# Performance work log

Hardware: AMD Instinct MI355X
Metric: run time of the kernel (lower is better)

## Reference

```python
import jax, jax.numpy as jnp
import numpy as np

NEG_SLOPE = 0.1
BN_EPS = 1e-5
STD_EPS = 1e-5


def leaky_relu(x):
    return jnp.where(x >= 0, x, NEG_SLOPE * x)


def conv_bn_act(x, w, gamma, beta):
    # Conv1d(kernel_size=1, bias=False) + BatchNorm1d (train-mode batch stats) + LeakyReLU(0.1)
    y = jnp.einsum('bcn,oc->bon', x, w)
    m = y.mean(axis=(0, 2), keepdims=True)
    v = y.var(axis=(0, 2), keepdims=True)  # biased, as torch BN
    y = (y - m) / jnp.sqrt(v + BN_EPS) * gamma[None, :, None] + beta[None, :, None]
    return leaky_relu(y)


def knn_idx(x, k):
    # x: [B, C, N]; faithful to torch knn(): topk(k+1) of negative squared distance, then keep first k (includes self)
    xx = jnp.sum(x * x, axis=1, keepdims=True)            # [B, 1, N]
    inner = -2.0 * jnp.einsum('bcn,bcm->bnm', x, x)       # [B, N, N]
    pd = -xx - inner - jnp.swapaxes(xx, 1, 2)             # [B, N, N]
    _, idx = jax.lax.top_k(pd, k + 1)
    return idx[:, :, :k]


def setup_inputs() -> dict:
    key = jax.random.key(0)
    ks = jax.random.split(key, 4)
    B, C, N, O = 8, 3, 4096, 32
    return {
        'xyz': jax.random.normal(ks[0], (B, C, N), dtype=jnp.float32),
        'w_nn': jax.random.normal(ks[1], (O, C), dtype=jnp.float32) * 0.1,
        'alpha': jnp.ones((1, 1, 1, O), dtype=jnp.float32),
        'beta_a': jnp.zeros((1, 1, 1, O), dtype=jnp.float32),
        'w0': jax.random.normal(ks[2], (O, C), dtype=jnp.float32) * 0.1,
        'g0': jnp.ones((O,), dtype=jnp.float32),
        'b0': jnp.zeros((O,), dtype=jnp.float32),
        'w1': jax.random.normal(ks[3], (O, O), dtype=jnp.float32) * 0.1,
        'g1': jnp.ones((O,), dtype=jnp.float32),
        'b1': jnp.zeros((O,), dtype=jnp.float32),
        'k': 16,
    }


def reference(xyz, w_nn, alpha, beta_a, w0, g0, b0, w1, g1, b1, k):
    # MLP branch on raw channels
    x = conv_bn_act(xyz, w0, g0, b0)
    x = conv_bn_act(x, w1, g1, b1)          # [B, 32, N]

    # KNN + gather neighbors
    idx = knn_idx(xyz, k)                   # [B, N, k]
    pts = jnp.swapaxes(xyz, 1, 2)           # [B, N, C]
    grouped = jax.vmap(lambda p, i: p[i])(pts, idx)  # [B, N, k, C]

    # neighbor_normal: diff -> 1x1 conv -> global-std normalize -> affine
    res = grouped - pts[:, :, None, :]
    res = jnp.einsum('bnkc,oc->bnko', res, w_nn)      # [B, N, k, 32]
    B = res.shape[0]
    std = jnp.std(res.reshape(B, -1), axis=-1, ddof=1).reshape(B, 1, 1, 1)  # torch.std is unbiased
    gp = alpha * (res / (std + STD_EPS)) + beta_a

    # max over neighbors, to [B, 32, N]
    gp = jnp.swapaxes(gp.max(axis=2), 1, 2)

    point_feature = jnp.concatenate([x, gp], axis=1)  # [B, 64, N]
    return point_feature, idx
```

## Files before the change

### kernel.cpp

```cpp
#include <hip/hip_runtime.h>
#include <stdint.h>

#define B_  8
#define N_  4096
#define O_  32
#define K_  16
#define BN_ (B_ * N_)
#define PF_ (B_ * 64 * N_)
#define CB_ 256
#define RPB 4
#define CHK 512
#define NCHK (N_ / CHK)

enum : int {
  WS_PARTA = 0,
  WS_XX    = 1024,
  WS_SC0   = WS_XX + BN_,
  WS_SH0   = WS_SC0 + 32,
  WS_PARTC = WS_SH0 + 32,
  WS_SC1   = WS_PARTC + 4096,
  WS_SH1   = WS_SC1 + 32,
  WS_MAXV  = WS_SH1 + 32,
  WS_MINV  = WS_MAXV + BN_ * 32,
  WS_ROWS  = WS_MINV + BN_ * 32,
  WS_DEN   = WS_ROWS + BN_ * 2,
  WS_TOTAL = WS_DEN + 8
};
#define WS_PARTC2 WS_MAXV

__global__ __launch_bounds__(256) void kA(const float* __restrict__ xyz,
                                          float* __restrict__ ws) {
  int tid = threadIdx.x;
  int gid = blockIdx.x * 256 + tid;
  float s0 = 0.f, s1 = 0.f, s2 = 0.f;
  float m00 = 0.f, m01 = 0.f, m02 = 0.f, m11 = 0.f, m12 = 0.f, m22 = 0.f;
  for (int i = gid; i < BN_; i += 64 * 256) {
    int b = i >> 12, n = i & (N_ - 1);
    const float* xb = xyz + b * 3 * N_;
    float x0 = xb[n], x1 = xb[N_ + n], x2 = xb[2 * N_ + n];
    float xx = __fadd_rn(__fadd_rn(__fmul_rn(x0, x0), __fmul_rn(x1, x1)),
                         __fmul_rn(x2, x2));
    ws[WS_XX + i] = xx;
    s0 += x0; s1 += x1; s2 += x2;
    m00 = fmaf(x0, x0, m00); m01 = fmaf(x0, x1, m01); m02 = fmaf(x0, x2, m02);
    m11 = fmaf(x1, x1, m11); m12 = fmaf(x1, x2, m12); m22 = fmaf(x2, x2, m22);
  }
  __shared__ float sd[256];
  float acc[9] = {s0, s1, s2, m00, m01, m02, m11, m12, m22};
#pragma unroll
  for (int q = 0; q < 9; ++q) {
    sd[tid] = acc[q];
    __syncthreads();
    for (int s = 128; s > 0; s >>= 1) {
      if (tid < s) sd[tid] += sd[tid + s];
      __syncthreads();
    }
    if (tid == 0) ws[WS_PARTA + blockIdx.x * 9 + q] = sd[0];
    __syncthreads();
  }
}

__global__ __launch_bounds__(64) void kB(const float* __restrict__ w0,
                                         const float* __restrict__ g0,
                                         const float* __restrict__ b0,
                                         float* __restrict__ ws) {
  __shared__ float S[9];
  int tid = threadIdx.x;
  if (tid < 9) {
    float s = 0.f;
    for (int blk = 0; blk < 64; ++blk) s += ws[WS_PARTA + blk * 9 + tid];
    S[tid] = s;
  }
  __syncthreads();
  if (tid < 32) {
    const float inv = 1.0f / 32768.0f;
    float mc0 = S[0] * inv, mc1 = S[1] * inv, mc2 = S[2] * inv;
    float M00 = S[3] * inv, M01 = S[4] * inv, M02 = S[5] * inv;
    float M11 = S[6] * inv, M12 = S[7] * inv, M22 = S[8] * inv;
    float w0c = w0[tid * 3], w1c = w0[tid * 3 + 1], w2c = w0[tid * 3 + 2];
    float m = w0c * mc0 + w1c * mc1 + w2c * mc2;
    float e2 = w0c * w0c * M00 + w1c * w1c * M11 + w2c * w2c * M22 +
               2.f * (w0c * w1c * M01 + w0c * w2c * M02 + w1c * w2c * M12);
    float v = fmaxf(e2 - m * m, 0.f);
    float sc = g0[tid] / sqrtf(v + 1e-5f);
    ws[WS_SC0 + tid] = sc;
    ws[WS_SH0 + tid] = b0[tid] - m * sc;
  }
}

__global__ __launch_bounds__(256) void kC(const float* __restrict__ xyz,
                                          const float* __restrict__ w0,
                                          const float* __restrict__ w1,
                                          float* __restrict__ ws) {
  __shared__ float w0s[96], sc0s[32], sh0s[32], w1s[32 * 33], xs[8][33], red[256];
  int tid = threadIdx.x;
  if (tid < 96) w0s[tid] = w0[tid];
  if (tid < 32) { sc0s[tid] = ws[WS_SC0 + tid]; sh0s[tid] = ws[WS_SH0 + tid]; }
  for (int i = tid; i < 1024; i += 256) w1s[(i >> 5) * 33 + (i & 31)] = w1[i];
  __syncthreads();
  int p = tid >> 5, o = tid & 31;
  float S = 0.f, S2 = 0.f;
  for (int it = 0; it < 16; ++it) {
    int i = blockIdx.x * 128 + it * 8 + p;
    int b = i >> 12, n = i & (N_ - 1);
    const float* xb = xyz + b * 3 * N_;
    float x0 = xb[n], x1 = xb[N_ + n], x2 = xb[2 * N_ + n];
    float y0 = x0 * w0s[o * 3] + x1 * w0s[o * 3 + 1] + x2 * w0s[o * 3 + 2];
    float a = y0 * sc0s[o] + sh0s[o];
    xs[p][o] = (a >= 0.f) ? a : 0.1f * a;
    __syncthreads();
    float y1 = 0.f;
#pragma unroll
    for (int c = 0; c < 32; ++c) y1 = fmaf(w1s[o * 33 + c], xs[p][c], y1);
    S += y1; S2 = fmaf(y1, y1, S2);
    __syncthreads();
  }
  red[tid] = S;
  __syncthreads();
  if (p == 0) {
    float t = 0.f;
    for (int pp = 0; pp < 8; ++pp) t += red[pp * 32 + o];
    ws[WS_PARTC2 + blockIdx.x * 64 + o] = t;
  }
  __syncthreads();
  red[tid] = S2;
  __syncthreads();
  if (p == 0) {
    float t = 0.f;
    for (int pp = 0; pp < 8; ++pp) t += red[pp * 32 + o];
    ws[WS_PARTC2 + blockIdx.x * 64 + 32 + o] = t;
  }
}

__global__ __launch_bounds__(64) void kD(const float* __restrict__ g1,
                                         const float* __restrict__ b1,
                                         float* __restrict__ ws) {
  int o = threadIdx.x;
  if (o >= 32) return;
  float S = 0.f, S2 = 0.f;
  for (int blk = 0; blk < CB_; ++blk) {
    S += ws[WS_PARTC2 + blk * 64 + o];
    S2 += ws[WS_PARTC2 + blk * 64 + 32 + o];
  }
  float m = S / 32768.f;
  float v = fmaxf(S2 / 32768.f - m * m, 0.f);
  float sc = g1[o] / sqrtf(v + 1e-5f);
  ws[WS_SC1 + o] = sc;
  ws[WS_SH1 + o] = b1[o] - m * sc;
}

__global__ __launch_bounds__(256) void kE(const float* __restrict__ xyz,
                                          const float* __restrict__ w0,
                                          const float* __restrict__ w1,
                                          const float* __restrict__ ws,
                                          float* __restrict__ out) {
  __shared__ float w0s[96], sc0s[32], sh0s[32], sc1s[32], sh1s[32], w1s[32 * 33],
      xs[8][33];
  int tid = threadIdx.x;
  if (tid < 96) w0s[tid] = w0[tid];
  if (tid < 32) {
    sc0s[tid] = ws[WS_SC0 + tid]; sh0s[tid] = ws[WS_SH0 + tid];
    sc1s[tid] = ws[WS_SC1 + tid]; sh1s[tid] = ws[WS_SH1 + tid];
  }
  for (int i = tid; i < 1024; i += 256) w1s[(i >> 5) * 33 + (i & 31)] = w1[i];
  __syncthreads();
  int p = tid >> 5, o = tid & 31;
  int o2 = tid >> 3, p2 = tid & 7;
  for (int it = 0; it < 16; ++it) {
    int i = blockIdx.x * 128 + it * 8 + p;
    int b = i >> 12, n = i & (N_ - 1);
    const float* xb = xyz + b * 3 * N_;
    float x0 = xb[n], x1 = xb[N_ + n], x2 = xb[2 * N_ + n];
    float y0 = x0 * w0s[o * 3] + x1 * w0s[o * 3 + 1] + x2 * w0s[o * 3 + 2];
    float a = y0 * sc0s[o] + sh0s[o];
    xs[p][o] = (a >= 0.f) ? a : 0.1f * a;
    __syncthreads();
    float y1 = 0.f;
#pragma unroll
    for (int c = 0; c < 32; ++c) y1 = fmaf(w1s[o * 33 + c], xs[p][c], y1);
    float z = y1 * sc1s[o] + sh1s[o];
    float x1v = (z >= 0.f) ? z : 0.1f * z;
    __syncthreads();
    xs[p][o] = x1v;
    __syncthreads();
    int i2 = blockIdx.x * 128 + it * 8 + p2;
    int b2 = i2 >> 12, n2 = i2 & (N_ - 1);
    out[b2 * 64 * N_ + o2 * N_ + n2] = xs[p2][o2];
    __syncthreads();
  }
}

__global__ __launch_bounds__(256) void kF(const float* __restrict__ xyz,
                                          const float* __restrict__ w_nn,
                                          float* __restrict__ out,
                                          float* __restrict__ ws) {
  int tid = threadIdx.x;
  int wave = tid >> 6, lane = tid & 63;
  int row = blockIdx.x * RPB + wave;
  int b = row >> 12, n = row & (N_ - 1);
  const float* xb = xyz + b * 3 * N_;
  const float* xxp = ws + WS_XX + b * N_;
  float qx = xb[n], qy = xb[N_ + n], qz = xb[2 * N_ + n];
  float xxn = xxp[n];

  __shared__ float sx[2][CHK], sy[2][CHK], sz[2][CHK], sxx[2][CHK];
  __shared__ unsigned long long list[RPB][64];
  __shared__ float rb[RPB][16][33];

  float keys[64];
  float mn = __builtin_inff();
  float rx0, rx1, ry0, ry1, rz0, rz1, rw0, rw1;
  rx0 = xb[tid];           rx1 = xb[tid + 256];
  ry0 = xb[N_ + tid];      ry1 = xb[N_ + tid + 256];
  rz0 = xb[2 * N_ + tid];  rz1 = xb[2 * N_ + tid + 256];
  rw0 = xxp[tid];          rw1 = xxp[tid + 256];
#pragma unroll
  for (int c = 0; c < NCHK; ++c) {
    int buf = c & 1;
    sx[buf][tid] = rx0;  sx[buf][tid + 256] = rx1;
    sy[buf][tid] = ry0;  sy[buf][tid + 256] = ry1;
    sz[buf][tid] = rz0;  sz[buf][tid + 256] = rz1;
    sxx[buf][tid] = rw0; sxx[buf][tid + 256] = rw1;
    __syncthreads();
    if (c + 1 < NCHK) {
      int i0 = (c + 1) * CHK + tid;
      rx0 = xb[i0];           rx1 = xb[i0 + 256];
      ry0 = xb[N_ + i0];      ry1 = xb[N_ + i0 + 256];
      rz0 = xb[2 * N_ + i0];  rz1 = xb[2 * N_ + i0 + 256];
      rw0 = xxp[i0];          rw1 = xxp[i0 + 256];
    }
#pragma unroll
    for (int jj = 0; jj < CHK / 64; ++jj) {
      int ml = (jj << 6) | lane;
      float px = sx[buf][ml], py = sy[buf][ml], pz = sz[buf][ml];
      float dot = __fmaf_rn(pz, qz, __fmaf_rn(py, qy, __fmul_rn(px, qx)));
      float inner = __fmul_rn(-2.0f, dot);
      float t = __fsub_rn(-sxx[buf][ml], inner);
      float pn = __fsub_rn(xxn, t);
      keys[c * (CHK / 64) + jj] = pn;
      mn = fminf(mn, pn);
    }
    __syncthreads();
  }

  unsigned e;
  {
    unsigned u = __float_as_uint(mn);
    u ^= ((unsigned)((int)u >> 31)) | 0x80000000u;
    e = u;
  }
#pragma unroll
  for (int k = 2; k <= 64; k <<= 1) {
#pragma unroll
    for (int d = k >> 1; d >= 1; d >>= 1) {
      unsigned pe = __shfl_xor(e, d, 64);
      bool up = ((lane & k) == 0);
      bool lower = ((lane & d) == 0);
      unsigned lo = (e < pe) ? e : pe;
      unsigned hi = (e < pe) ? pe : e;
      e = (up == lower) ? lo : hi;
    }
  }
  unsigned tm = __shfl(e, 15, 64);
  unsigned tfu = (tm & 0x80000000u) ? (tm ^ 0x80000000u) : ~tm;
  float T = __uint_as_float(tfu);

  list[wave][lane] = ~0ull;
  __syncthreads();
  int base = 0;
#pragma unroll
  for (int j = 0; j < 64; ++j) {
    bool pred = (keys[j] <= T);
    unsigned long long mask = __ballot(pred);
    if (mask != 0ull) {
      if (pred) {
        unsigned uu = __float_as_uint(keys[j]);
        uu ^= ((unsigned)((int)uu >> 31)) | 0x80000000u;
        int rank = __popcll(mask & ((1ull << lane) - 1ull));
        int slot = base + rank;
        if (slot < 64)
          list[wave][slot] = ((unsigned long long)uu << 32) |
                             (unsigned)((j << 6) | lane);
      }
      base += __popcll(mask);
    }
  }
  __syncthreads();

  unsigned long long ev = list[wave][lane];
#pragma unroll
  for (int k = 2; k <= 64; k <<= 1) {
#pragma unroll
    for (int d = k >> 1; d >= 1; d >>= 1) {
      unsigned long long pe = __shfl_xor(ev, d, 64);
      bool up = ((lane & k) == 0);
      bool lower = ((lane & d) == 0);
      bool lt = (ev < pe);
      unsigned long long lo = lt ? ev : pe;
      unsigned long long hi = lt ? pe : ev;
      ev = (up == lower) ? lo : hi;
    }
  }
  int m = (int)(unsigned)(ev & 0xffffffffull);
  if (lane < 16) out[PF_ + row * 16 + lane] = (float)m;

  float s = 0.f, s2 = 0.f;
  if (lane < 16) {
    float dx = __fsub_rn(xb[m], qx);
    float dy = __fsub_rn(xb[N_ + m], qy);
    float dz = __fsub_rn(xb[2 * N_ + m], qz);
#pragma unroll
    for (int o = 0; o < 32; ++o) {
      float r = __fmaf_rn(dz, w_nn[o * 3 + 2],
                __fmaf_rn(dy, w_nn[o * 3 + 1], __fmul_rn(dx, w_nn[o * 3])));
      rb[wave][lane][o] = r;
      s += r;
      s2 = __fmaf_rn(r, r, s2);
    }
  }
  __syncthreads();
  if (lane < 32) {
    float mx = -__builtin_inff(), mnv = __builtin_inff();
#pragma unroll
    for (int r = 0; r < 16; ++r) {
      float v = rb[wave][r][lane];
      mx = fmaxf(mx, v);
      mnv = fminf(mnv, v);
    }
    ws[WS_MAXV + row * 32 + lane] = mx;
    ws[WS_MINV + row * 32 + lane] = mnv;
  }
#pragma unroll
  for (int off = 1; off < 64; off <<= 1) {
    s += __shfl_xor(s, off, 64);
    s2 += __shfl_xor(s2, off, 64);
  }
  if (lane == 0) {
    ws[WS_ROWS + row * 2] = s;
    ws[WS_ROWS + row * 2 + 1] = s2;
  }
}

__global__ __launch_bounds__(256) void kG(float* __restrict__ ws) {
  int b = blockIdx.x, tid = threadIdx.x;
  float s = 0.f, s2 = 0.f;
  for (int i = tid; i < N_; i += 256) {
    s += ws[WS_ROWS + (b * N_ + i) * 2];
    s2 += ws[WS_ROWS + (b * N_ + i) * 2 + 1];
  }
  __shared__ float sd[256], sd2[256];
  sd[tid] = s; sd2[tid] = s2;
  __syncthreads();
  for (int st = 128; st > 0; st >>= 1) {
    if (tid < st) { sd[tid] += sd[tid + st]; sd2[tid] += sd2[tid + st]; }
    __syncthreads();
  }
  if (tid == 0) {
    const float M = 2097152.0f;
    float var = fmaxf((sd2[0] - sd[0] * (sd[0] / M)) / (M - 1.0f), 0.f);
    ws[WS_DEN + b] = sqrtf(var) + 1e-5f;
  }
}

__global__ __launch_bounds__(256) void kH(const float* __restrict__ alpha,
                                          const float* __restrict__ beta,
                                          const float* __restrict__ ws,
                                          float* __restrict__ out) {
  int i = blockIdx.x * 256 + threadIdx.x;
  if (i >= B_ * 32 * N_) return;
  int n = i & (N_ - 1);
  int o = (i >> 12) & 31;
  int b = i >> 17;
  float denom = ws[WS_DEN + b];
  float al = alpha[o], be = beta[o];
  int base = (b * N_ + n) * 32 + o;
  float v = (al >= 0.f) ? ws[WS_MAXV + base] : ws[WS_MINV + base];
  out[b * 64 * N_ + (32 + o) * N_ + n] = __fadd_rn(__fmul_rn(al, v / denom), be);
}

extern "C" void kernel_launch(void* const* d_in, const int* in_sizes, int n_in,
                              void* d_out, int out_size, void* d_ws, size_t ws_size,
                              hipStream_t stream) {
  const float* xyz   = (const float*)d_in[0];
  const float* w_nn  = (const float*)d_in[1];
  const float* alpha = (const float*)d_in[2];
  const float* beta_a= (const float*)d_in[3];
  const float* w0    = (const float*)d_in[4];
  const float* g0    = (const float*)d_in[5];
  const float* b0    = (const float*)d_in[6];
  const float* w1    = (const float*)d_in[7];
  const float* g1    = (const float*)d_in[8];
  const float* b1    = (const float*)d_in[9];
  float* out = (float*)d_out;
  float* ws  = (float*)d_ws;

  kA<<<64, 256, 0, stream>>>(xyz, ws);
  kB<<<1, 64, 0, stream>>>(w0, g0, b0, ws);
  kC<<<CB_, 256, 0, stream>>>(xyz, w0, w1, ws);
  kD<<<1, 64, 0, stream>>>(g1, b1, ws);
  kE<<<CB_, 256, 0, stream>>>(xyz, w0, w1, ws, out);
  kF<<<BN_ / RPB, RPB * 64, 0, stream>>>(xyz, w_nn, out, ws);
  kG<<<B_, 256, 0, stream>>>(ws);
  kH<<<(B_ * 32 * N_ + 255) / 256, 256, 0, stream>>>(alpha, beta_a, ws, out);
}
```

Baseline: 155.9 us.

## Fold tiny reduction kernels into consumers and process two KNN rows per wave

Removes the single-block kernels kB, kD and kG by having each consuming block recompute the BN scale/shift or the per-batch std from the partial sums, cutting launch count from eight to five. The KNN kernel now handles two query rows per wave (RPB 8 with 256 threads), so each shared-memory candidate point is reused for two distance computations. The cost is redundant reduction work in every block of kC, kE and kH, and doubled key registers per lane (128 floats), which may lower occupancy or cause spills.

Result: slower. 187.3 us (+20.1%).

```diff
diff --git a/kernel.cpp b/kernel.cpp
--- a/kernel.cpp
+++ b/kernel.cpp
@@ -8,7 +8,7 @@
 #define BN_ (B_ * N_)
 #define PF_ (B_ * 64 * N_)
 #define CB_ 256
-#define RPB 4
+#define RPB 8
 #define CHK 512
 #define NCHK (N_ / CHK)
 
@@ -60,43 +60,38 @@
   }
 }
 
-__global__ __launch_bounds__(64) void kB(const float* __restrict__ w0,
-                                         const float* __restrict__ g0,
-                                         const float* __restrict__ b0,
-                                         float* __restrict__ ws) {
-  __shared__ float S[9];
+__global__ __launch_bounds__(256) void kC(const float* __restrict__ xyz,
+                                          const float* __restrict__ w0,
+                                          const float* __restrict__ g0,
+                                          const float* __restrict__ b0,
+                                          const float* __restrict__ w1,
+                                          float* __restrict__ ws) {
+  __shared__ float S9[9];
+  __shared__ float w0s[96], sc0s[32], sh0s[32], w1s[32 * 33], xs[8][33], red[256];
   int tid = threadIdx.x;
   if (tid < 9) {
     float s = 0.f;
     for (int blk = 0; blk < 64; ++blk) s += ws[WS_PARTA + blk * 9 + tid];
-    S[tid] = s;
-  }
+    S9[tid] = s;
+  }
+  if (tid < 96) w0s[tid] = w0[tid];
+  for (int i = tid; i < 1024; i += 256) w1s[(i >> 5) * 33 + (i & 31)] = w1[i];
   __syncthreads();
   if (tid < 32) {
     const float inv = 1.0f / 32768.0f;
-    float mc0 = S[0] * inv, mc1 = S[1] * inv, mc2 = S[2] * inv;
-    float M00 = S[3] * inv, M01 = S[4] * inv, M02 = S[5] * inv;
-    float M11 = S[6] * inv, M12 = S[7] * inv, M22 = S[8] * inv;
+    float mc0 = S9[0] * inv, mc1 = S9[1] * inv, mc2 = S9[2] * inv;
+    float M00 = S9[3] * inv, M01 = S9[4] * inv, M02 = S9[5] * inv;
+    float M11 = S9[6] * inv, M12 = S9[7] * inv, M22 = S9[8] * inv;
     float w0c = w0[tid * 3], w1c = w0[tid * 3 + 1], w2c = w0[tid * 3 + 2];
     float m = w0c * mc0 + w1c * mc1 + w2c * mc2;
     float e2 = w0c * w0c * M00 + w1c * w1c * M11 + w2c * w2c * M22 +
                2.f * (w0c * w1c * M01 + w0c * w2c * M02 + w1c * w2c * M12);
     float v = fmaxf(e2 - m * m, 0.f);
     float sc = g0[tid] / sqrtf(v + 1e-5f);
-    ws[WS_SC0 + tid] = sc;
-    ws[WS_SH0 + tid] = b0[tid] - m * sc;
-  }
-}
-
-__global__ __launch_bounds__(256) void kC(const float* __restrict__ xyz,
-                                          const float* __restrict__ w0,
-                                          const float* __restrict__ w1,
-                                          float* __restrict__ ws) {
-  __shared__ float w0s[96], sc0s[32], sh0s[32], w1s[32 * 33], xs[8][33], red[256];
-  int tid = threadIdx.x;
-  if (tid < 96) w0s[tid] = w0[tid];
-  if (tid < 32) { sc0s[tid] = ws[WS_SC0 + tid]; sh0s[tid] = ws[WS_SH0 + tid]; }
-  for (int i = tid; i < 1024; i += 256) w1s[(i >> 5) * 33 + (i & 31)] = w1[i];
+    float sh = b0[tid] - m * sc;
+    sc0s[tid] = sc; sh0s[tid] = sh;
+    if (blockIdx.x == 0) { ws[WS_SC0 + tid] = sc; ws[WS_SH0 + tid] = sh; }
+  }
   __syncthreads();
   int p = tid >> 5, o = tid & 31;
   float S = 0.f, S2 = 0.f;
@@ -132,26 +127,11 @@
   }
 }
 
-__global__ __launch_bounds__(64) void kD(const float* __restrict__ g1,
-                                         const float* __restrict__ b1,
-                                         float* __restrict__ ws) {
-  int o = threadIdx.x;
-  if (o >= 32) return;
-  float S = 0.f, S2 = 0.f;
-  for (int blk = 0; blk < CB_; ++blk) {
-    S += ws[WS_PARTC2 + blk * 64 + o];
-    S2 += ws[WS_PARTC2 + blk * 64 + 32 + o];
-  }
-  float m = S / 32768.f;
-  float v = fmaxf(S2 / 32768.f - m * m, 0.f);
-  float sc = g1[o] / sqrtf(v + 1e-5f);
-  ws[WS_SC1 + o] = sc;
-  ws[WS_SH1 + o] = b1[o] - m * sc;
-}
-
 __global__ __launch_bounds__(256) void kE(const float* __restrict__ xyz,
                                           const float* __restrict__ w0,
                                           const float* __restrict__ w1,
+                                          const float* __restrict__ g1,
+                                          const float* __restrict__ b1,
                                           const float* __restrict__ ws,
                                           float* __restrict__ out) {
   __shared__ float w0s[96], sc0s[32], sh0s[32], sc1s[32], sh1s[32], w1s[32 * 33],
@@ -160,7 +140,15 @@
   if (tid < 96) w0s[tid] = w0[tid];
   if (tid < 32) {
     sc0s[tid] = ws[WS_SC0 + tid]; sh0s[tid] = ws[WS_SH0 + tid];
-    sc1s[tid] = ws[WS_SC1 + tid]; sh1s[tid] = ws[WS_SH1 + tid];
+    float S = 0.f, S2 = 0.f;
+    for (int blk = 0; blk < CB_; ++blk) {
+      S += ws[WS_PARTC2 + blk * 64 + tid];
+      S2 += ws[WS_PARTC2 + blk * 64 + 32 + tid];
+    }
+    float m = S / 32768.f;
+    float v = fmaxf(S2 / 32768.f - m * m, 0.f);
+    float sc = g1[tid] / sqrtf(v + 1e-5f);
+    sc1s[tid] = sc; sh1s[tid] = b1[tid] - m * sc;
   }
   for (int i = tid; i < 1024; i += 256) w1s[(i >> 5) * 33 + (i & 31)] = w1[i];
   __syncthreads();
@@ -196,19 +184,20 @@
                                           float* __restrict__ ws) {
   int tid = threadIdx.x;
   int wave = tid >> 6, lane = tid & 63;
-  int row = blockIdx.x * RPB + wave;
-  int b = row >> 12, n = row & (N_ - 1);
+  int row0 = blockIdx.x * RPB + wave * 2;
+  int b = row0 >> 12;
   const float* xb = xyz + b * 3 * N_;
   const float* xxp = ws + WS_XX + b * N_;
-  float qx = xb[n], qy = xb[N_ + n], qz = xb[2 * N_ + n];
-  float xxn = xxp[n];
+  int n0 = row0 & (N_ - 1), n1 = n0 + 1;
+  float qx0 = xb[n0], qy0 = xb[N_ + n0], qz0 = xb[2 * N_ + n0], xxn0 = xxp[n0];
+  float qx1 = xb[n1], qy1 = xb[N_ + n1], qz1 = xb[2 * N_ + n1], xxn1 = xxp[n1];
 
   __shared__ float sx[2][CHK], sy[2][CHK], sz[2][CHK], sxx[2][CHK];
   __shared__ unsigned long long list[RPB][64];
   __shared__ float rb[RPB][16][33];
 
-  float keys[64];
-  float mn = __builtin_inff();
+  float keys[2][64];
+  float mn0 = __builtin_inff(), mn1 = __builtin_inff();
   float rx0, rx1, ry0, ry1, rz0, rz1, rw0, rw1;
   rx0 = xb[tid];           rx1 = xb[tid + 256];
   ry0 = xb[N_ + tid];      ry1 = xb[N_ + tid + 256];
@@ -233,132 +222,127 @@
     for (int jj = 0; jj < CHK / 64; ++jj) {
       int ml = (jj << 6) | lane;
       float px = sx[buf][ml], py = sy[buf][ml], pz = sz[buf][ml];
-      float dot = __fmaf_rn(pz, qz, __fmaf_rn(py, qy, __fmul_rn(px, qx)));
-      float inner = __fmul_rn(-2.0f, dot);
-      float t = __fsub_rn(-sxx[buf][ml], inner);
-      float pn = __fsub_rn(xxn, t);
-      keys[c * (CHK / 64) + jj] = pn;
-      mn = fminf(mn, pn);
-    }
-    __syncthreads();
-  }
-
-  unsigned e;
-  {
-    unsigned u = __float_as_uint(mn);
-    u ^= ((unsigned)((int)u >> 31)) | 0x80000000u;
-    e = u;
-  }
-#pragma unroll
-  for (int k = 2; k <= 64; k <<= 1) {
-#pragma unroll
-    for (int d = k >> 1; d >= 1; d >>= 1) {
-      unsigned pe = __shfl_xor(e, d, 64);
-      bool up = ((lane & k) == 0);
-      bool lower = ((lane & d) == 0);
-      unsigned lo = (e < pe) ? e : pe;
-      unsigned hi = (e < pe) ? pe : e;
-      e = (up == lower) ? lo : hi;
-    }
-  }
-  unsigned tm = __shfl(e, 15, 64);
-  unsigned tfu = (tm & 0x80000000u) ? (tm ^ 0x80000000u) : ~tm;
-  float T = __uint_as_float(tfu);
-
-  list[wave][lane] = ~0ull;
-  __syncthreads();
-  int base = 0;
-#pragma unroll
-  for (int j = 0; j < 64; ++j) {
-    bool pred = (keys[j] <= T);
-    unsigned long long mask = __ballot(pred);
-    if (mask != 0ull) {
-      if (pred) {
-        unsigned uu = __float_as_uint(keys[j]);
-        uu ^= ((unsigned)((int)uu >> 31)) | 0x80000000u;
-        int rank = __popcll(mask & ((1ull << lane) - 1ull));
-        int slot = base + rank;
-        if (slot < 64)
-          list[wave][slot] = ((unsigned long long)uu << 32) |
+      float pw = sxx[buf][ml];
+      float dot0 = __fmaf_rn(pz, qz0, __fmaf_rn(py, qy0, __fmul_rn(px, qx0)));
+      float in0 = __fmul_rn(-2.0f, dot0);
+      float t0 = __fsub_rn(-pw, in0);
+      float pn0 = __fsub_rn(xxn0, t0);
+      keys[0][c * (CHK / 64) + jj] = pn0;
+      mn0 = fminf(mn0, pn0);
+      float dot1 = __fmaf_rn(pz, qz1, __fmaf_rn(py, qy1, __fmul_rn(px, qx1)));
+      float in1 = __fmul_rn(-2.0f, dot1);
+      float t1 = __fsub_rn(-pw, in1);
+      float pn1 = __fsub_rn(xxn1, t1);
+      keys[1][c * (CHK / 64) + jj] = pn1;
+      mn1 = fminf(mn1, pn1);
+    }
+    __syncthreads();
+  }
+
+#pragma unroll
+  for (int rr = 0; rr < 2; ++rr) {
+    int row = row0 + rr;
+    int lw = wave * 2 + rr;
+    float mn = rr ? mn1 : mn0;
+
+    unsigned e;
+    {
+      unsigned u = __float_as_uint(mn);
+      u ^= ((unsigned)((int)u >> 31)) | 0x80000000u;
+      e = u;
+    }
+#pragma unroll
+    for (int k = 2; k <= 64; k <<= 1) {
+#pragma unroll
+      for (int d = k >> 1; d >= 1; d >>= 1) {
+        unsigned pe = __shfl_xor(e, d, 64);
+        bool up = ((lane & k) == 0);
+        bool lower = ((lane & d) == 0);
+        unsigned lo = (e < pe) ? e : pe;
+        unsigned hi = (e < pe) ? pe : e;
+        e = (up == lower) ? lo : hi;
+      }
+    }
+    unsigned tm = __shfl(e, 15, 64);
+    unsigned tfu = (tm & 0x80000000u) ? (tm ^ 0x80000000u) : ~tm;
+    float T = __uint_as_float(tfu);
+
+    list[lw][lane] = ~0ull;
+    __syncthreads();
+    int base = 0;
+#pragma unroll
+    for (int j = 0; j < 64; ++j) {
+      bool pred = (keys[rr][j] <= T);
+      unsigned long long mask = __ballot(pred);
+      if (mask != 0ull) {
+        if (pred) {
+          unsigned uu = __float_as_uint(keys[rr][j]);
+          uu ^= ((unsigned)((int)uu >> 31)) | 0x80000000u;
+          int rank = __popcll(mask & ((1ull << lane) - 1ull));
+          int slot = base + rank;
+          if (slot < 64)
+            list[lw][slot] = ((unsigned long long)uu << 32) |
                              (unsigned)((j << 6) | lane);
+        }
+        base += __popcll(mask);
       }
-      base += __popcll(mask);
-    }
-  }
-  __syncthreads();
-
-  unsigned long long ev = list[wave][lane];
-#pragma unroll
-  for (int k = 2; k <= 64; k <<= 1) {
-#pragma unroll
-    for (int d = k >> 1; d >= 1; d >>= 1) {
-      unsigned long long pe = __shfl_xor(ev, d, 64);
-      bool up = ((lane & k) == 0);
-      bool lower = ((lane & d) == 0);
-      bool lt = (ev < pe);
-      unsigned long long lo = lt ? ev : pe;
-      unsigned long long hi = lt ? pe : ev;
-      ev = (up == lower) ? lo : hi;
-    }
-  }
-  int m = (int)(unsigned)(ev & 0xffffffffull);
-  if (lane < 16) out[PF_ + row * 16 + lane] = (float)m;
-
-  float s = 0.f, s2 = 0.f;
-  if (lane < 16) {
-    float dx = __fsub_rn(xb[m], qx);
-    float dy = __fsub_rn(xb[N_ + m], qy);
-    float dz = __fsub_rn(xb[2 * N_ + m], qz);
-#pragma unroll
-    for (int o = 0; o < 32; ++o) {
-      float r = __fmaf_rn(dz, w_nn[o * 3 + 2],
-                __fmaf_rn(dy, w_nn[o * 3 + 1], __fmul_rn(dx, w_nn[o * 3])));
-      rb[wave][lane][o] = r;
-      s += r;
-      s2 = __fmaf_rn(r, r, s2);
-    }
-  }
-  __syncthreads();
-  if (lane < 32) {
-    float mx = -__builtin_inff(), mnv = __builtin_inff();
-#pragma unroll
-    for (int r = 0; r < 16; ++r) {
-      float v = rb[wave][r][lane];
-      mx = fmaxf(mx, v);
-      mnv = fminf(mnv, v);
-    }
-    ws[WS_MAXV + row * 32 + lane] = mx;
-    ws[WS_MINV + row * 32 + lane] = mnv;
-  }
-#pragma unroll
-  for (int off = 1; off < 64; off <<= 1) {
-    s += __shfl_xor(s, off, 64);
-    s2 += __shfl_xor(s2, off, 64);
-  }
-  if (lane == 0) {
-    ws[WS_ROWS + row * 2] = s;
-    ws[WS_ROWS + row * 2 + 1] = s2;
-  }
-}
-
-__global__ __launch_bounds__(256) void kG(float* __restrict__ ws) {
-  int b = blockIdx.x, tid = threadIdx.x;
-  float s = 0.f, s2 = 0.f;
-  for (int i = tid; i < N_; i += 256) {
-    s += ws[WS_ROWS + (b * N_ + i) * 2];
-    s2 += ws[WS_ROWS + (b * N_ + i) * 2 + 1];
-  }
-  __shared__ float sd[256], sd2[256];
-  sd[tid] = s; sd2[tid] = s2;
-  __syncthreads();
-  for (int st = 128; st > 0; st >>= 1) {
-    if (tid < st) { sd[tid] += sd[tid + st]; sd2[tid] += sd2[tid + st]; }
-    __syncthreads();
-  }
-  if (tid == 0) {
-    const float M = 2097152.0f;
-    float var = fmaxf((sd2[0] - sd[0] * (sd[0] / M)) / (M - 1.0f), 0.f);
-    ws[WS_DEN + b] = sqrtf(var) + 1e-5f;
+    }
+    __syncthreads();
+
+    unsigned long long ev = list[lw][lane];
+#pragma unroll
+    for (int k = 2; k <= 64; k <<= 1) {
+#pragma unroll
+      for (int d = k >> 1; d >= 1; d >>= 1) {
+        unsigned long long pe = __shfl_xor(ev, d, 64);
+        bool up = ((lane & k) == 0);
+        bool lower = ((lane & d) == 0);
+        bool lt = (ev < pe);
+        unsigned long long lo = lt ? ev : pe;
+        unsigned long long hi = lt ? pe : ev;
+        ev = (up == lower) ? lo : hi;
+      }
+    }
+    int m = (int)(unsigned)(ev & 0xffffffffull);
+    if (lane < 16) out[PF_ + row * 16 + lane] = (float)m;
+
+    float qx = rr ? qx1 : qx0, qy = rr ? qy1 : qy0, qz = rr ? qz1 : qz0;
+    float s = 0.f, s2 = 0.f;
+    if (lane < 16) {
+      float dx = __fsub_rn(xb[m], qx);
+      float dy = __fsub_rn(xb[N_ + m], qy);
+      float dz = __fsub_rn(xb[2 * N_ + m], qz);
+#pragma unroll
+      for (int o = 0; o < 32; ++o) {
+        float r = __fmaf_rn(dz, w_nn[o * 3 + 2],
+                  __fmaf_rn(dy, w_nn[o * 3 + 1], __fmul_rn(dx, w_nn[o * 3])));
+        rb[lw][lane][o] = r;
+        s += r;
+        s2 = __fmaf_rn(r, r, s2);
+      }
+    }
+    __syncthreads();
+    if (lane < 32) {
+      float mx = -__builtin_inff(), mnv = __builtin_inff();
+#pragma unroll
+      for (int r = 0; r < 16; ++r) {
+        float v = rb[lw][r][lane];
+        mx = fmaxf(mx, v);
+        mnv = fminf(mnv, v);
+      }
+      ws[WS_MAXV + row * 32 + lane] = mx;
+      ws[WS_MINV + row * 32 + lane] = mnv;
+    }
+#pragma unroll
+    for (int off = 1; off < 64; off <<= 1) {
+      s += __shfl_xor(s, off, 64);
+      s2 += __shfl_xor(s2, off, 64);
+    }
+    if (lane == 0) {
+      ws[WS_ROWS + row * 2] = s;
+      ws[WS_ROWS + row * 2 + 1] = s2;
+    }
+    __syncthreads();
   }
 }
 
@@ -366,12 +350,31 @@
                                           const float* __restrict__ beta,
                                           const float* __restrict__ ws,
                                           float* __restrict__ out) {
-  int i = blockIdx.x * 256 + threadIdx.x;
-  if (i >= B_ * 32 * N_) return;
+  int tid = threadIdx.x;
+  int i = blockIdx.x * 256 + tid;
+  int b = i >> 17;
+  float s = 0.f, s2 = 0.f;
+  for (int q = tid; q < N_; q += 256) {
+    s += ws[WS_ROWS + (b * N_ + q) * 2];
+    s2 += ws[WS_ROWS + (b * N_ + q) * 2 + 1];
+  }
+  __shared__ float sd[256], sd2[256];
+  __shared__ float den_s;
+  sd[tid] = s; sd2[tid] = s2;
+  __syncthreads();
+  for (int st = 128; st > 0; st >>= 1) {
+    if (tid < st) { sd[tid] += sd[tid + st]; sd2[tid] += sd2[tid + st]; }
+    __syncthreads();
+  }
+  if (tid == 0) {
+    const float M = 2097152.0f;
+    float var = fmaxf((sd2[0] - sd[0] * (sd[0] / M)) / (M - 1.0f), 0.f);
+    den_s = sqrtf(var) + 1e-5f;
+  }
+  __syncthreads();
+  float denom = den_s;
   int n = i & (N_ - 1);
   int o = (i >> 12) & 31;
-  int b = i >> 17;
-  float denom = ws[WS_DEN + b];
   float al = alpha[o], be = beta[o];
   int base = (b * N_ + n) * 32 + o;
   float v = (al >= 0.f) ? ws[WS_MAXV + base] : ws[WS_MINV + base];
@@ -395,11 +398,8 @@
   float* ws  = (float*)d_ws;
 
   kA<<<64, 256, 0, stream>>>(xyz, ws);
-  kB<<<1, 64, 0, stream>>>(w0, g0, b0, ws);
-  kC<<<CB_, 256, 0, stream>>>(xyz, w0, w1, ws);
-  kD<<<1, 64, 0, stream>>>(g1, b1, ws);
-  kE<<<CB_, 256, 0, stream>>>(xyz, w0, w1, ws, out);
-  kF<<<BN_ / RPB, RPB * 64, 0, stream>>>(xyz, w_nn, out, ws);
-  kG<<<B_, 256, 0, stream>>>(ws);
+  kC<<<CB_, 256, 0, stream>>>(xyz, w0, g0, b0, w1, ws);
+  kE<<<CB_, 256, 0, stream>>>(xyz, w0, w1, g1, b1, ws, out);
+  kF<<<BN_ / RPB, 256, 0, stream>>>(xyz, w_nn, out, ws);
   kH<<<(B_ * 32 * N_ + 255) / 256, 256, 0, stream>>>(alpha, beta_a, ws, out);
 }
```
